# Performance work log

Hardware: AMD Instinct MI355X
Metric: run time of the kernel (lower is better)

Reference implementation:

```python
import jax, jax.numpy as jnp
import numpy as np

HIDDEN = 256
MAX_POS = 2000  # table has MAX_POS + 1 rows


def get_sinusoid_encoding_table(n_position, d_hid):
    pos = np.arange(n_position, dtype=np.float64)[:, None]
    i = np.arange(d_hid)[None, :]
    angle = pos / np.power(10000.0, 2.0 * (i // 2) / d_hid)
    table = np.zeros((n_position, d_hid), dtype=np.float32)
    table[:, 0::2] = np.sin(angle[:, 0::2])
    table[:, 1::2] = np.cos(angle[:, 1::2])
    return jnp.asarray(table)


def setup_inputs() -> dict:
    key = jax.random.key(0)
    k1, k2 = jax.random.split(key)
    B, T = 64, 160
    x = jax.random.normal(k1, (B, T, HIDDEN), dtype=jnp.float32)
    duration = jax.random.randint(k2, (B, T), 0, 12, dtype=jnp.int64 if jax.config.jax_enable_x64 else jnp.int32)
    position_enc = get_sinusoid_encoding_table(MAX_POS + 1, HIDDEN)
    return {"x": x, "position_enc": position_enc, "duration": duration, "max_len": 2000}


def reference(x, position_enc, duration, max_len):
    # x: [B, T, H], duration: [B, T] ints, max_len: python int
    B, T, H = x.shape
    csum = jnp.cumsum(duration, axis=1)            # inclusive cumsum [B, T]
    excl = csum - duration                          # exclusive cumsum [B, T]
    mel_len = csum[:, -1]                           # [B]
    frames = jnp.arange(max_len)                    # [L]
    # token index owning each output frame: smallest t with csum[t] > frame
    idx = jax.vmap(lambda c: jnp.searchsorted(c, frames, side='right'))(csum)  # [B, L]
    idx = jnp.minimum(idx, T - 1)
    valid = frames[None, :] < mel_len[:, None]      # [B, L]
    # gather expanded features
    out = jnp.take_along_axis(x, idx[..., None], axis=1)          # [B, L, H]
    # per-token local position -> sinusoid table row
    pos_within = frames[None, :] - jnp.take_along_axis(excl, idx, axis=1)  # [B, L]
    pos_within = jnp.where(valid, pos_within, 0)
    pos = position_enc[pos_within]                                 # [B, L, H]
    out = jnp.where(valid[..., None], out, 0.0)
    pos = jnp.where(valid[..., None], pos, 0.0)
    return out, pos, mel_len
```

## Files before the change

### kernel.cpp

```cpp
#include <hip/hip_runtime.h>

constexpr int B      = 64;
constexpr int T      = 160;
constexpr int H      = 256;
constexpr int MAXLEN = 2000;
constexpr int FPB    = 16;
constexpr int NTH    = 256;

__global__ __launch_bounds__(NTH) void lr_kernel(
    const float* __restrict__ x,
    const float* __restrict__ pos_enc,
    const int*   __restrict__ duration,
    float*       __restrict__ out)
{
    __shared__ int s_scan[NTH];
    __shared__ int s_map[FPB];
    __shared__ int s_mel;

    const int b   = blockIdx.y;
    const int tid = threadIdx.x;
    const int f0  = blockIdx.x * FPB;

    int d = (tid < T) ? duration[b * T + tid] : 0;
    s_scan[tid] = d;
    if (tid < FPB) s_map[tid] = -1;
    __syncthreads();
    #pragma unroll
    for (int off = 1; off < NTH; off <<= 1) {
        int v   = s_scan[tid];
        int add = (tid >= off) ? s_scan[tid - off] : 0;
        __syncthreads();
        s_scan[tid] = v + add;
        __syncthreads();
    }
    const int csum = s_scan[tid];
    if (tid == T - 1) s_mel = csum;

    if (tid < T && d > 0) {
        const int start = csum - d;
        const int lo = max(start, f0);
        const int hi = min(csum, f0 + FPB);
        for (int f = lo; f < hi; ++f)
            s_map[f - f0] = (tid << 4) | (f - start);
    }
    __syncthreads();

    if (blockIdx.x == 0 && tid == 0) {
        out[(size_t)2 * B * MAXLEN * H + b] = (float)s_mel;
    }

    const int wave = tid >> 6;
    const int lane = tid & 63;

    const float4* __restrict__ x4 = (const float4*)x;
    const float4* __restrict__ p4 = (const float4*)pos_enc;
    float4* __restrict__ o4 = (float4*)out;

    const size_t out_base = (size_t)b * MAXLEN * (H / 4);
    const size_t pos_base = (size_t)B * MAXLEN * (H / 4) + out_base;

    float4 xo[4], po[4];
    #pragma unroll
    for (int i = 0; i < 4; ++i) {
        const int m = s_map[wave + i * 4];
        xo[i] = make_float4(0.f, 0.f, 0.f, 0.f);
        po[i] = xo[i];
        if (m >= 0) {
            const int idx = m >> 4;
            const int pw  = m & 15;
            xo[i] = x4[((size_t)b * T + idx) * (H / 4) + lane];
            po[i] = p4[(size_t)pw * (H / 4) + lane];
        }
    }
    #pragma unroll
    for (int i = 0; i < 4; ++i) {
        const int f = f0 + wave + i * 4;
        o4[out_base + (size_t)f * (H / 4) + lane] = xo[i];
        o4[pos_base + (size_t)f * (H / 4) + lane] = po[i];
    }
}

extern "C" void kernel_launch(void* const* d_in, const int* in_sizes, int n_in,
                              void* d_out, int out_size, void* d_ws, size_t ws_size,
                              hipStream_t stream)
{
    const float* x        = (const float*)d_in[0];
    const float* pos_enc  = (const float*)d_in[1];
    const int*   duration = (const int*)d_in[2];
    float*       out      = (float*)d_out;

    dim3 grid(MAXLEN / FPB, B);
    lr_kernel<<<grid, NTH, 0, stream>>>(x, pos_enc, duration, out);
}
```

Baseline: 269.1 us.

## Split prefix scan into separate kernel writing frame-to-token map

Moves the per-batch duration prefix scan out of the expansion kernel into a small kernel that runs once per batch row and writes a frame-to-token map into workspace. The expansion kernel then reads its 16 map entries directly instead of redoing a 256-thread scan with 8 barrier rounds in each of 125 blocks per row. This adds a second launch and a global-memory round trip for the map, plus a serial dependency between the two kernels.

Measured after the change: 271.0 us (median of 2 runs). About the same (+0.7%).

```diff
diff --git a/kernel.cpp b/kernel.cpp
--- a/kernel.cpp
+++ b/kernel.cpp
@@ -7,23 +7,18 @@
 constexpr int FPB    = 16;
 constexpr int NTH    = 256;
 
-__global__ __launch_bounds__(NTH) void lr_kernel(
-    const float* __restrict__ x,
-    const float* __restrict__ pos_enc,
-    const int*   __restrict__ duration,
-    float*       __restrict__ out)
+__global__ __launch_bounds__(NTH) void lr_scan_kernel(
+    const int* __restrict__ duration,
+    int*       __restrict__ map,
+    float*     __restrict__ out)
 {
     __shared__ int s_scan[NTH];
-    __shared__ int s_map[FPB];
-    __shared__ int s_mel;
 
-    const int b   = blockIdx.y;
+    const int b   = blockIdx.x;
     const int tid = threadIdx.x;
-    const int f0  = blockIdx.x * FPB;
 
     int d = (tid < T) ? duration[b * T + tid] : 0;
     s_scan[tid] = d;
-    if (tid < FPB) s_map[tid] = -1;
     __syncthreads();
     #pragma unroll
     for (int off = 1; off < NTH; off <<= 1) {
@@ -34,23 +29,34 @@
         __syncthreads();
     }
     const int csum = s_scan[tid];
-    if (tid == T - 1) s_mel = csum;
+    const int mel  = s_scan[T - 1];
+
+    int* mrow = map + b * MAXLEN;
 
     if (tid < T && d > 0) {
         const int start = csum - d;
-        const int lo = max(start, f0);
-        const int hi = min(csum, f0 + FPB);
-        for (int f = lo; f < hi; ++f)
-            s_map[f - f0] = (tid << 4) | (f - start);
+        for (int f = start; f < csum; ++f)
+            mrow[f] = (tid << 4) | (f - start);
     }
-    __syncthreads();
+    for (int f = mel + tid; f < MAXLEN; f += NTH)
+        mrow[f] = -1;
 
-    if (blockIdx.x == 0 && tid == 0) {
-        out[(size_t)2 * B * MAXLEN * H + b] = (float)s_mel;
-    }
+    if (tid == 0)
+        out[(size_t)2 * B * MAXLEN * H + b] = (float)mel;
+}
 
-    const int wave = tid >> 6;
-    const int lane = tid & 63;
+__global__ __launch_bounds__(NTH) void lr_expand_kernel(
+    const float* __restrict__ x,
+    const float* __restrict__ pos_enc,
+    const int*   __restrict__ map,
+    float*       __restrict__ out)
+{
+    const int b    = blockIdx.y;
+    const int f0   = blockIdx.x * FPB;
+    const int wave = threadIdx.x >> 6;
+    const int lane = threadIdx.x & 63;
+
+    const int* __restrict__ mrow = map + b * MAXLEN + f0;
 
     const float4* __restrict__ x4 = (const float4*)x;
     const float4* __restrict__ p4 = (const float4*)pos_enc;
@@ -59,15 +65,18 @@
     const size_t out_base = (size_t)b * MAXLEN * (H / 4);
     const size_t pos_base = (size_t)B * MAXLEN * (H / 4) + out_base;
 
+    int m[4];
+    #pragma unroll
+    for (int i = 0; i < 4; ++i) m[i] = mrow[wave + i * 4];
+
     float4 xo[4], po[4];
     #pragma unroll
     for (int i = 0; i < 4; ++i) {
-        const int m = s_map[wave + i * 4];
         xo[i] = make_float4(0.f, 0.f, 0.f, 0.f);
         po[i] = xo[i];
-        if (m >= 0) {
-            const int idx = m >> 4;
-            const int pw  = m & 15;
+        if (m[i] >= 0) {
+            const int idx = m[i] >> 4;
+            const int pw  = m[i] & 15;
             xo[i] = x4[((size_t)b * T + idx) * (H / 4) + lane];
             po[i] = p4[(size_t)pw * (H / 4) + lane];
         }
@@ -88,7 +97,10 @@
     const float* pos_enc  = (const float*)d_in[1];
     const int*   duration = (const int*)d_in[2];
     float*       out      = (float*)d_out;
+    int*         map      = (int*)d_ws;
+
+    lr_scan_kernel<<<B, NTH, 0, stream>>>(duration, map, out);
 
     dim3 grid(MAXLEN / FPB, B);
-    lr_kernel<<<grid, NTH, 0, stream>>>(x, pos_enc, duration, out);
+    lr_expand_kernel<<<grid, NTH, 0, stream>>>(x, pos_enc, map, out);
 }
```
